# Optimization experiments

Hardware: AMD Instinct MI355X
Metric: run time of the kernel (lower is better)

The kernel has to match this reference:

```python
import jax, jax.numpy as jnp
import numpy as np

GRID_H, GRID_W = 24, 24
N_BASE_ACTIONS = 6
B = 131072


def setup_inputs() -> dict:
    key = jax.random.key(0)
    k1, k2, k3 = jax.random.split(key, 3)
    logits = jax.random.normal(k1, (GRID_H, GRID_W), dtype=jnp.float32)
    monoaction_mask = jax.random.randint(k2, (B, GRID_H, GRID_W), 0, 2).astype(jnp.bool_)
    monofield_base_converter = jax.random.randint(k3, (GRID_H, GRID_W), 0, N_BASE_ACTIONS, dtype=jnp.int32)
    return {
        "logits": logits,
        "monoaction_mask": monoaction_mask,
        "monofield_base_converter": monofield_base_converter,
    }


def reference(logits, monoaction_mask, monofield_base_converter):
    # scale: divide sap action (last) by 225
    scale = jnp.ones((1, N_BASE_ACTIONS), dtype=jnp.float32).at[:, -1].set(225.0)
    # one-hot grouping of grid cells into base actions: (H, W, N)
    onehot = (monofield_base_converter[..., None]
              == jnp.arange(N_BASE_ACTIONS, dtype=jnp.int32)).astype(logits.dtype)
    m = monoaction_mask.astype(logits.dtype)  # (B, H, W)
    # grouped masked sum over grid, equivalent to sum(where=mask) in original
    masked_logits = jnp.einsum('bhw,hwn->bn', m * logits[None, :, :], onehot)  # (B, N)
    counts = jnp.einsum('bhw,hwn->bn', m, onehot)  # (B, N)
    any_mask = counts > 0  # == jnp.any(mask, axis=(-3,-2)) in original
    masked_logits = masked_logits / scale
    masked_logits = jnp.where(any_mask, masked_logits, jnp.finfo(jnp.float32).min)
    # if no valid cell at all for this unit, force logit[0] = 1.0
    any_unit = jnp.any(monoaction_mask, axis=(-2, -1))  # (B,)
    masked_logits = jnp.where(any_unit[..., None], masked_logits,
                              masked_logits.at[..., 0].set(1.0))
    return masked_logits
```

## Files before the change

kernel.cpp:

```cpp
#include <hip/hip_runtime.h>


typedef short bf16x8 __attribute__((ext_vector_type(8)));
typedef float f32x4 __attribute__((ext_vector_type(4)));
typedef unsigned uint4n __attribute__((ext_vector_type(4)));

union U4S8 { uint4n u; bf16x8 s; };

__device__ inline unsigned short f2bf(float f) {
  unsigned u = __builtin_bit_cast(unsigned, f);
  u += 0x7FFFu + ((u >> 16) & 1u);
  return (unsigned short)(u >> 16);
}

__global__ void build_wt_kernel(const float* __restrict__ logits,
                                const int* __restrict__ conv,
                                const unsigned* __restrict__ mask_dw,
                                unsigned short* __restrict__ wt_perm,
                                unsigned short* __restrict__ wt_id,
                                int* __restrict__ flag) {
  if (blockIdx.x == 0) {
    unsigned long long bad = __ballot(mask_dw[threadIdx.x] > 1u);
    __shared__ int votes[4];
    if ((threadIdx.x & 63) == 0) votes[threadIdx.x >> 6] = (bad != 0ull);
    __syncthreads();
    if (threadIdx.x == 0)
      *flag = !(votes[0] | votes[1] | votes[2] | votes[3]);
  }
  int idx = blockIdx.x * blockDim.x + threadIdx.x;
  if (idx >= 16 * 576) return;
  int n = idx / 576;
  int cell = idx - n * 576;
  int g = conv[cell];
  unsigned short v = 0;
  if (n < 6)        v = (g == n)       ? f2bf(logits[cell]) : (unsigned short)0;
  else if (n < 12)  v = (g == (n - 6)) ? (unsigned short)0x3F80 : (unsigned short)0;
  else if (n == 12) v = 0x3F80;
  wt_id[n * 576 + cell] = v;
  int jp = cell & 7, q = (cell >> 4) & 3, sub = (cell >> 3) & 1, kt = cell >> 6;
  int j = (jp & 4) | ((jp & 1) << 1) | ((jp & 2) >> 1);
  wt_perm[n * 576 + kt * 64 + sub * 32 + q * 8 + j] = v;
}

__device__ inline void cvt_pair(unsigned x, unsigned& lo, unsigned& hi) {
  lo = (x & 0x00010001u) * 0x3F80u;
  hi = ((x >> 8) & 0x00010001u) * 0x3F80u;
}

__global__ __launch_bounds__(256) void head_kernel(
    const unsigned char* __restrict__ mask,
    const unsigned short* __restrict__ wt_perm,
    const unsigned short* __restrict__ wt_id,
    const int* __restrict__ flag,
    float* __restrict__ out,
    int ntiles) {
  int gid  = blockIdx.x * blockDim.x + threadIdx.x;
  int wave = gid >> 6;
  int lane = threadIdx.x & 63;
  if (wave >= ntiles) return;

  int m = lane & 15;
  int q = lane >> 4;
  size_t tb = (size_t)wave * 16;

  f32x4 acc = {0.f, 0.f, 0.f, 0.f};

  if (*flag) {
    const unsigned* mp = (const unsigned*)mask + (tb + (size_t)m) * 576 + q * 8;
    const unsigned char* bp = (const unsigned char*)wt_id + m * 1152 + q * 16;
#pragma unroll 3
    for (int kt = 0; kt < 18; ++kt) {
      uint4n u = __builtin_nontemporal_load((const uint4n*)(mp + kt * 32));
      uint4n w = __builtin_nontemporal_load((const uint4n*)(mp + kt * 32 + 4));
      U4S8 a, b;
      b.u = *(const uint4n*)(bp + kt * 64);
      a.u = (uint4n){(u.x | (u.y << 16)) * 0x3F80u,
                     (u.z | (u.w << 16)) * 0x3F80u,
                     (w.x | (w.y << 16)) * 0x3F80u,
                     (w.z | (w.w << 16)) * 0x3F80u};
      acc = __builtin_amdgcn_mfma_f32_16x16x32_bf16(a.s, b.s, acc, 0, 0, 0);
    }
  } else {
    const unsigned char* ap = mask + (tb + (size_t)m) * 576 + q * 16;
    const unsigned char* bp = (const unsigned char*)wt_perm + m * 1152 + q * 16;
#pragma unroll 3
    for (int kt = 0; kt < 9; ++kt) {
      uint4n av = __builtin_nontemporal_load((const uint4n*)(ap + kt * 64));
      U4S8 a0, a1, b0, b1;
      b0.u = *(const uint4n*)(bp + kt * 128);
      b1.u = *(const uint4n*)(bp + kt * 128 + 64);
      unsigned l0, h0, l1, h1;
      cvt_pair(av.x, l0, h0); cvt_pair(av.y, l1, h1);
      a0.u = (uint4n){l0, h0, l1, h1};
      cvt_pair(av.z, l0, h0); cvt_pair(av.w, l1, h1);
      a1.u = (uint4n){l0, h0, l1, h1};
      acc = __builtin_amdgcn_mfma_f32_16x16x32_bf16(a0.s, b0.s, acc, 0, 0, 0);
      acc = __builtin_amdgcn_mfma_f32_16x16x32_bf16(a1.s, b1.s, acc, 0, 0, 0);
    }
  }

  int col = m;
  int srcCnt = (lane & 48) + ((col < 6) ? (col + 6) : 0);
  int srcTot = (lane & 48) + 12;
  float scale = (col == 5) ? (1.0f / 225.0f) : 1.0f;
  const float FMIN = -3.4028234663852886e38f;

#pragma unroll
  for (int r = 0; r < 4; ++r) {
    float s   = acc[r];
    float cnt = __shfl(s, srcCnt);
    float tot = __shfl(s, srcTot);
    if (col < 6) {
      float o;
      if (tot < 0.5f)       o = (col == 0) ? 1.0f : FMIN;
      else if (cnt > 0.5f)  o = s * scale;
      else                  o = FMIN;
      size_t b = tb + (size_t)q * 4 + r;
      out[b * 6 + col] = o;
    }
  }
}

extern "C" void kernel_launch(void* const* d_in, const int* in_sizes, int n_in,
                              void* d_out, int out_size, void* d_ws, size_t ws_size,
                              hipStream_t stream) {
  const float*          logits = (const float*)d_in[0];
  const unsigned char*  mask   = (const unsigned char*)d_in[1];
  const int*            conv   = (const int*)d_in[2];
  float*                out    = (float*)d_out;

  int*            flag    = (int*)d_ws;
  unsigned short* wt_perm = (unsigned short*)((char*)d_ws + 64);
  unsigned short* wt_id   = wt_perm + 16 * 576;

  int B = in_sizes[1] / 576;
  int ntiles = B / 16;

  build_wt_kernel<<<36, 256, 0, stream>>>(logits, conv, (const unsigned*)mask,
                                          wt_perm, wt_id, flag);

  int threads = ntiles * 64;
  head_kernel<<<(threads + 255) / 256, 256, 0, stream>>>(
      mask, wt_perm, wt_id, flag, out, ntiles);
}
```

Before: 394.6 us.

## Fuse weight-table build into head kernel using per-block LDS weights

```diff
diff --git a/kernel.cpp b/kernel.cpp
--- a/kernel.cpp
+++ b/kernel.cpp
@@ -13,33 +13,14 @@
   return (unsigned short)(u >> 16);
 }
 
-__global__ void build_wt_kernel(const float* __restrict__ logits,
-                                const int* __restrict__ conv,
-                                const unsigned* __restrict__ mask_dw,
-                                unsigned short* __restrict__ wt_perm,
-                                unsigned short* __restrict__ wt_id,
-                                int* __restrict__ flag) {
-  if (blockIdx.x == 0) {
-    unsigned long long bad = __ballot(mask_dw[threadIdx.x] > 1u);
-    __shared__ int votes[4];
-    if ((threadIdx.x & 63) == 0) votes[threadIdx.x >> 6] = (bad != 0ull);
-    __syncthreads();
-    if (threadIdx.x == 0)
-      *flag = !(votes[0] | votes[1] | votes[2] | votes[3]);
-  }
-  int idx = blockIdx.x * blockDim.x + threadIdx.x;
-  if (idx >= 16 * 576) return;
-  int n = idx / 576;
-  int cell = idx - n * 576;
+__device__ inline unsigned short wval(const float* __restrict__ logits,
+                                      const int* __restrict__ conv,
+                                      int cell, int n) {
+  if (n > 12) return 0;
+  if (n == 12) return 0x3F80;
   int g = conv[cell];
-  unsigned short v = 0;
-  if (n < 6)        v = (g == n)       ? f2bf(logits[cell]) : (unsigned short)0;
-  else if (n < 12)  v = (g == (n - 6)) ? (unsigned short)0x3F80 : (unsigned short)0;
-  else if (n == 12) v = 0x3F80;
-  wt_id[n * 576 + cell] = v;
-  int jp = cell & 7, q = (cell >> 4) & 3, sub = (cell >> 3) & 1, kt = cell >> 6;
-  int j = (jp & 4) | ((jp & 1) << 1) | ((jp & 2) >> 1);
-  wt_perm[n * 576 + kt * 64 + sub * 32 + q * 8 + j] = v;
+  if (n < 6) return (g == n) ? f2bf(logits[cell]) : (unsigned short)0;
+  return (g == n - 6) ? (unsigned short)0x3F80 : (unsigned short)0;
 }
 
 __device__ inline void cvt_pair(unsigned x, unsigned& lo, unsigned& hi) {
@@ -48,54 +29,82 @@
 }
 
 __global__ __launch_bounds__(256) void head_kernel(
+    const float* __restrict__ logits,
     const unsigned char* __restrict__ mask,
-    const unsigned short* __restrict__ wt_perm,
-    const unsigned short* __restrict__ wt_id,
-    const int* __restrict__ flag,
+    const int* __restrict__ conv,
     float* __restrict__ out,
     int ntiles) {
-  int gid  = blockIdx.x * blockDim.x + threadIdx.x;
-  int wave = gid >> 6;
-  int lane = threadIdx.x & 63;
-  if (wave >= ntiles) return;
+  __shared__ __align__(16) unsigned short wt[18 * 64 * 8];
+  __shared__ int votes[4];
+
+  int tid = threadIdx.x;
+  const unsigned* mask_dw = (const unsigned*)mask;
+
+  unsigned long long bad = __ballot(mask_dw[tid] > 1u);
+  if ((tid & 63) == 0) votes[tid >> 6] = (bad != 0ull);
+  __syncthreads();
+  int flag = !(votes[0] | votes[1] | votes[2] | votes[3]);
+
+  if (flag) {
+#pragma unroll 2
+    for (int i = 0; i < 36; ++i) {
+      int e = tid + i * 256;
+      int j = e & 7, l = (e >> 3) & 63, kt = e >> 9;
+      int cell = kt * 32 + (l >> 4) * 8 + j;
+      wt[e] = wval(logits, conv, cell, l & 15);
+    }
+  } else {
+#pragma unroll 2
+    for (int i = 0; i < 36; ++i) {
+      int e = tid + i * 256;
+      int j = e & 7, l = (e >> 3) & 63, f = e >> 9;
+      int pj = (j & 4) | ((j & 1) << 1) | ((j & 2) >> 1);
+      int cell = (f >> 1) * 64 + (l >> 4) * 16 + (f & 1) * 8 + pj;
+      wt[e] = wval(logits, conv, cell, l & 15);
+    }
+  }
+  __syncthreads();
+
+  int lane = tid & 63;
+  int tile = blockIdx.x * 4 + (tid >> 6);
+  if (tile >= ntiles) return;
 
   int m = lane & 15;
   int q = lane >> 4;
-  size_t tb = (size_t)wave * 16;
+  size_t tb = (size_t)tile * 16;
+  const bf16x8* wl = (const bf16x8*)wt;
 
   f32x4 acc = {0.f, 0.f, 0.f, 0.f};
 
-  if (*flag) {
-    const unsigned* mp = (const unsigned*)mask + (tb + (size_t)m) * 576 + q * 8;
-    const unsigned char* bp = (const unsigned char*)wt_id + m * 1152 + q * 16;
+  if (flag) {
+    const unsigned* mp = mask_dw + (tb + (size_t)m) * 576 + q * 8;
 #pragma unroll 3
     for (int kt = 0; kt < 18; ++kt) {
       uint4n u = __builtin_nontemporal_load((const uint4n*)(mp + kt * 32));
       uint4n w = __builtin_nontemporal_load((const uint4n*)(mp + kt * 32 + 4));
-      U4S8 a, b;
-      b.u = *(const uint4n*)(bp + kt * 64);
+      U4S8 a;
       a.u = (uint4n){(u.x | (u.y << 16)) * 0x3F80u,
                      (u.z | (u.w << 16)) * 0x3F80u,
                      (w.x | (w.y << 16)) * 0x3F80u,
                      (w.z | (w.w << 16)) * 0x3F80u};
-      acc = __builtin_amdgcn_mfma_f32_16x16x32_bf16(a.s, b.s, acc, 0, 0, 0);
+      acc = __builtin_amdgcn_mfma_f32_16x16x32_bf16(a.s, wl[kt * 64 + lane],
+                                                    acc, 0, 0, 0);
     }
   } else {
     const unsigned char* ap = mask + (tb + (size_t)m) * 576 + q * 16;
-    const unsigned char* bp = (const unsigned char*)wt_perm + m * 1152 + q * 16;
 #pragma unroll 3
     for (int kt = 0; kt < 9; ++kt) {
       uint4n av = __builtin_nontemporal_load((const uint4n*)(ap + kt * 64));
-      U4S8 a0, a1, b0, b1;
-      b0.u = *(const uint4n*)(bp + kt * 128);
-      b1.u = *(const uint4n*)(bp + kt * 128 + 64);
+      U4S8 a0, a1;
       unsigned l0, h0, l1, h1;
       cvt_pair(av.x, l0, h0); cvt_pair(av.y, l1, h1);
       a0.u = (uint4n){l0, h0, l1, h1};
       cvt_pair(av.z, l0, h0); cvt_pair(av.w, l1, h1);
       a1.u = (uint4n){l0, h0, l1, h1};
-      acc = __builtin_amdgcn_mfma_f32_16x16x32_bf16(a0.s, b0.s, acc, 0, 0, 0);
-      acc = __builtin_amdgcn_mfma_f32_16x16x32_bf16(a1.s, b1.s, acc, 0, 0, 0);
+      acc = __builtin_amdgcn_mfma_f32_16x16x32_bf16(a0.s, wl[(2 * kt) * 64 + lane],
+                                                    acc, 0, 0, 0);
+      acc = __builtin_amdgcn_mfma_f32_16x16x32_bf16(a1.s, wl[(2 * kt + 1) * 64 + lane],
+                                                    acc, 0, 0, 0);
     }
   }
 
@@ -129,17 +138,9 @@
   const int*            conv   = (const int*)d_in[2];
   float*                out    = (float*)d_out;
 
-  int*            flag    = (int*)d_ws;
-  unsigned short* wt_perm = (unsigned short*)((char*)d_ws + 64);
-  unsigned short* wt_id   = wt_perm + 16 * 576;
-
   int B = in_sizes[1] / 576;
   int ntiles = B / 16;
+  int blocks = (ntiles + 3) / 4;
 
-  build_wt_kernel<<<36, 256, 0, stream>>>(logits, conv, (const unsigned*)mask,
-                                          wt_perm, wt_id, flag);
-
-  int threads = ntiles * 64;
-  head_kernel<<<(threads + 255) / 256, 256, 0, stream>>>(
-      mask, wt_perm, wt_id, flag, out, ntiles);
+  head_kernel<<<blocks, 256, 0, stream>>>(logits, mask, conv, out, ntiles);
 }
```

After: 403.8 us. 2.3% more time.
